# Kernel optimization log

Hardware: AMD Instinct MI355X
Metric: run time of the kernel (lower is better)

## Reference

```python
import jax, jax.numpy as jnp
import numpy as np

NUM_CLASSES = 10


def _decode(out, thresh, anchors, stride):
    # out: [B, 45, H, W] -> [B, H, W, 3, 15]
    B, C, H, W = out.shape
    o = out.transpose(0, 2, 3, 1).reshape(B, H, W, 3, -1)
    mask = o[..., 0] > thresh                      # [B,H,W,3]
    ys = jnp.arange(H, dtype=o.dtype)[None, :, None, None]
    xs = jnp.arange(W, dtype=o.dtype)[None, None, :, None]
    pre_x = (xs + o[..., 1]) * stride
    pre_y = (ys + o[..., 2]) * stride
    iou = o[..., 0]
    kind = jnp.argmax(o[..., 5:5 + NUM_CLASSES], axis=-1).astype(o.dtype)
    pre_w = anchors[:, 0] * jnp.exp(o[..., 3])     # anchors broadcast over last (anchor) dim
    pre_h = anchors[:, 1] * jnp.exp(o[..., 4])
    x1 = pre_x - 0.5 * pre_w
    y1 = pre_y - 0.5 * pre_h
    x2 = pre_x + 0.5 * pre_w
    y2 = pre_y + 0.5 * pre_h
    boxes = jnp.stack([iou, x1, y1, x2, y2, kind], axis=-1)  # [B,H,W,3,6]
    return boxes.reshape(-1, 6), mask.reshape(-1)


def setup_inputs() -> dict:
    key = jax.random.key(0)
    k = jax.random.split(key, 6)
    return {
        "output13": jax.random.normal(k[0], (128, 45, 13, 13), dtype=jnp.float32),
        "output26": jax.random.normal(k[1], (128, 45, 26, 26), dtype=jnp.float32),
        "output52": jax.random.normal(k[2], (128, 45, 52, 52), dtype=jnp.float32),
        "anchors13": jax.random.uniform(k[3], (3, 2), dtype=jnp.float32),
        "anchors26": jax.random.uniform(k[4], (3, 2), dtype=jnp.float32),
        "anchors52": jax.random.uniform(k[5], (3, 2), dtype=jnp.float32),
        "thresh": jnp.zeros((), dtype=jnp.float32),
    }


def reference(output13, output26, output52, anchors13, anchors26, anchors52, thresh):
    # JIT-friendly dense equivalent of mask -> nonzero -> gather -> decode:
    # decode every (batch, cell, anchor) slot and return the compaction mask
    # alongside; the masked rows correspond exactly to torch's gathered rows.
    b13, m13 = _decode(output13, thresh, anchors13, 32.0)
    b26, m26 = _decode(output26, thresh, anchors26, 16.0)
    b52, m52 = _decode(output52, thresh, anchors52, 8.0)
    boxes = jnp.concatenate([b13, b26, b52], axis=0)  # [N_total, 6]
    mask = jnp.concatenate([m13, m26, m52], axis=0)   # [N_total]
    return boxes, mask
```

## Files before the change

### kernel.cpp

```cpp
#include <hip/hip_runtime.h>


constexpr int  BATCH = 128;
constexpr long N13 = 128L * 13 * 13 * 3;
constexpr long N26 = 128L * 26 * 26 * 3;
constexpr long N52 = 128L * 52 * 52 * 3;
constexpr long NTOT = N13 + N26 + N52;

constexpr int BLOCK = 256;
constexpr int T52 = 128 * 3 * (52 * 52 / 4);
constexpr int T26 = 128 * 3 * (26 * 26 / 4);
constexpr int T13 = (int)N13;
constexpr int B52 = (T52 + BLOCK - 1) / BLOCK;
constexpr int B26 = (T26 + BLOCK - 1) / BLOCK;
constexpr int B13 = (T13 + BLOCK - 1) / BLOCK;

template <int H, int STRIDE, long ROWOFF>
__device__ __forceinline__ void decode_vec(const float* __restrict__ o,
                                           const float* __restrict__ anc,
                                           float thresh,
                                           float* __restrict__ out, int tid)
{
    constexpr int hw = H * H;
    constexpr int C4 = hw / 4;
    constexpr int NT = BATCH * 3 * C4;
    if (tid >= NT) return;

    int a = tid % 3;
    int t = tid / 3;
    int chunk = t % C4;
    int b = t / C4;

    const float4* base = (const float4*)o + (b * 45 + a * 15) * C4 + chunk;

    float v[15][4];
#pragma unroll
    for (int j = 0; j < 15; ++j) {
        float4 q = base[j * C4];
        v[j][0] = q.x; v[j][1] = q.y; v[j][2] = q.z; v[j][3] = q.w;
    }

    float2 A = ((const float2*)anc)[a];

    int cell0 = chunk * 4;
    int x = cell0 % H;
    int y = cell0 / H;
    long row = ROWOFF + ((long)b * hw + cell0) * 3 + a;

#pragma unroll
    for (int i = 0; i < 4; ++i) {
        float iou = v[0][i];
        float px = ((float)x + v[1][i]) * (float)STRIDE;
        float py = ((float)y + v[2][i]) * (float)STRIDE;
        float pw = A.x * expf(v[3][i]);
        float ph = A.y * expf(v[4][i]);

        int kind = 0;
        float best = v[5][i];
#pragma unroll
        for (int c = 1; c < 10; ++c)
            if (v[5 + c][i] > best) { best = v[5 + c][i]; kind = c; }

        float2* orow = (float2*)out + row * 3;
        orow[0] = make_float2(iou, px - 0.5f * pw);
        orow[1] = make_float2(py - 0.5f * ph, px + 0.5f * pw);
        orow[2] = make_float2(py + 0.5f * ph, (float)kind);
        out[6 * NTOT + row] = (iou > thresh) ? 1.0f : 0.0f;

        row += 3;
        if (++x == H) { x = 0; ++y; }
    }
}

template <int H, int STRIDE, long ROWOFF>
__device__ __forceinline__ void decode_scalar(const float* __restrict__ o,
                                              const float* __restrict__ anc,
                                              float thresh,
                                              float* __restrict__ out, int tid)
{
    constexpr int hw = H * H;
    constexpr int NT = BATCH * hw * 3;
    if (tid >= NT) return;

    int a = tid % 3;
    int cell = tid / 3;
    int x = (cell % hw) % H;
    int y = (cell % hw) / H;
    int b = cell / hw;

    const float* p = o + (b * 45 + a * 15) * hw + y * H + x;

    float v[15];
#pragma unroll
    for (int j = 0; j < 15; ++j) v[j] = p[j * hw];

    float iou = v[0];
    float px = ((float)x + v[1]) * (float)STRIDE;
    float py = ((float)y + v[2]) * (float)STRIDE;
    float2 A = ((const float2*)anc)[a];
    float pw = A.x * expf(v[3]);
    float ph = A.y * expf(v[4]);

    int kind = 0;
    float best = v[5];
#pragma unroll
    for (int c = 1; c < 10; ++c)
        if (v[5 + c] > best) { best = v[5 + c]; kind = c; }

    long row = ROWOFF + tid;
    float2* orow = (float2*)out + row * 3;
    orow[0] = make_float2(iou, px - 0.5f * pw);
    orow[1] = make_float2(py - 0.5f * ph, px + 0.5f * pw);
    orow[2] = make_float2(py + 0.5f * ph, (float)kind);
    out[6 * NTOT + row] = (iou > thresh) ? 1.0f : 0.0f;
}

__global__ __launch_bounds__(256) void decode_all(
    const float* __restrict__ o13, const float* __restrict__ o26,
    const float* __restrict__ o52, const float* __restrict__ a13,
    const float* __restrict__ a26, const float* __restrict__ a52,
    const float* __restrict__ thr, float* __restrict__ out)
{
    const float thresh = *thr;
    int blk = blockIdx.x;
    if (blk < B52) {
        decode_vec<52, 8, N13 + N26>(o52, a52, thresh, out, blk * BLOCK + (int)threadIdx.x);
    } else if (blk < B52 + B26) {
        decode_vec<26, 16, N13>(o26, a26, thresh, out, (blk - B52) * BLOCK + (int)threadIdx.x);
    } else {
        decode_scalar<13, 32, 0L>(o13, a13, thresh, out, (blk - B52 - B26) * BLOCK + (int)threadIdx.x);
    }
}

extern "C" void kernel_launch(void* const* d_in, const int* in_sizes, int n_in,
                              void* d_out, int out_size, void* d_ws, size_t ws_size,
                              hipStream_t stream) {
    const float* o13 = (const float*)d_in[0];
    const float* o26 = (const float*)d_in[1];
    const float* o52 = (const float*)d_in[2];
    const float* a13 = (const float*)d_in[3];
    const float* a26 = (const float*)d_in[4];
    const float* a52 = (const float*)d_in[5];
    const float* thr = (const float*)d_in[6];
    float* out = (float*)d_out;

    decode_all<<<B52 + B26 + B13, BLOCK, 0, stream>>>(o13, o26, o52, a13, a26, a52, thr, out);
}
```

Measured before the change: 137.0 us.

## Stage decoded boxes in LDS and write them out with coalesced float4 stores

Each 192-thread block now covers 64 consecutive 4-cell chunks across all 3 anchors, with one wavefront per anchor. Boxes and mask values are staged in shared memory and then written back as contiguous float4 stores. This replaces the strided float2 and scalar global writes of the old layout. It adds a __syncthreads and about 21 KB of LDS per block, which may limit occupancy, and changes the block size and grid mapping so every block divides the problem exactly.

Result: faster. 126.7 us (-7.5%).

```diff
diff --git a/kernel.cpp b/kernel.cpp
--- a/kernel.cpp
+++ b/kernel.cpp
@@ -7,45 +7,47 @@
 constexpr long N52 = 128L * 52 * 52 * 3;
 constexpr long NTOT = N13 + N26 + N52;
 
-constexpr int BLOCK = 256;
-constexpr int T52 = 128 * 3 * (52 * 52 / 4);
-constexpr int T26 = 128 * 3 * (26 * 26 / 4);
-constexpr int T13 = (int)N13;
-constexpr int B52 = (T52 + BLOCK - 1) / BLOCK;
-constexpr int B26 = (T26 + BLOCK - 1) / BLOCK;
-constexpr int B13 = (T13 + BLOCK - 1) / BLOCK;
+constexpr int BLOCK = 192;
+constexpr int GC52 = 128 * (52 * 52 / 4);
+constexpr int GC26 = 128 * (26 * 26 / 4);
+constexpr int B52 = GC52 / 64;
+constexpr int B26 = GC26 / 64;
+constexpr int B13 = (int)N13 / BLOCK;
 
 template <int H, int STRIDE, long ROWOFF>
-__device__ __forceinline__ void decode_vec(const float* __restrict__ o,
-                                           const float* __restrict__ anc,
-                                           float thresh,
-                                           float* __restrict__ out, int tid)
+__device__ __forceinline__ void decode_vec_lds(const float* __restrict__ o,
+                                               const float* __restrict__ anc,
+                                               float thresh,
+                                               float* __restrict__ out, int blk)
 {
     constexpr int hw = H * H;
     constexpr int C4 = hw / 4;
-    constexpr int NT = BATCH * 3 * C4;
-    if (tid >= NT) return;
 
-    int a = tid % 3;
-    int t = tid / 3;
-    int chunk = t % C4;
-    int b = t / C4;
+    __shared__ float sbox[768 * 6];
+    __shared__ float smask[768];
 
-    const float4* base = (const float4*)o + (b * 45 + a * 15) * C4 + chunk;
+    const int lane = threadIdx.x & 63;
+    const int a    = threadIdx.x >> 6;
+    const int gc0  = blk * 64;
+    const int gc   = gc0 + lane;
+    const int b    = gc / C4;
+    const int chunk = gc % C4;
+
+    const float4* base = (const float4*)o + (long)(b * 45 + a * 15) * C4 + chunk;
 
     float v[15][4];
 #pragma unroll
     for (int j = 0; j < 15; ++j) {
-        float4 q = base[j * C4];
+        float4 q = base[(long)j * C4];
         v[j][0] = q.x; v[j][1] = q.y; v[j][2] = q.z; v[j][3] = q.w;
     }
 
-    float2 A = ((const float2*)anc)[a];
+    const float2 A = ((const float2*)anc)[a];
 
     int cell0 = chunk * 4;
     int x = cell0 % H;
     int y = cell0 / H;
-    long row = ROWOFF + ((long)b * hw + cell0) * 3 + a;
+    int lr = lane * 12 + a;
 
 #pragma unroll
     for (int i = 0; i < 4; ++i) {
@@ -61,15 +63,26 @@
         for (int c = 1; c < 10; ++c)
             if (v[5 + c][i] > best) { best = v[5 + c][i]; kind = c; }
 
-        float2* orow = (float2*)out + row * 3;
-        orow[0] = make_float2(iou, px - 0.5f * pw);
-        orow[1] = make_float2(py - 0.5f * ph, px + 0.5f * pw);
-        orow[2] = make_float2(py + 0.5f * ph, (float)kind);
-        out[6 * NTOT + row] = (iou > thresh) ? 1.0f : 0.0f;
+        float* r = &sbox[(lr + i * 3) * 6];
+        ((float2*)r)[0] = make_float2(iou, px - 0.5f * pw);
+        ((float2*)r)[1] = make_float2(py - 0.5f * ph, px + 0.5f * pw);
+        ((float2*)r)[2] = make_float2(py + 0.5f * ph, (float)kind);
+        smask[lr + i * 3] = (iou > thresh) ? 1.0f : 0.0f;
 
-        row += 3;
         if (++x == H) { x = 0; ++y; }
     }
+
+    __syncthreads();
+
+    const long row0 = ROWOFF + (long)gc0 * 12;
+    const float4* sb = (const float4*)sbox;
+    float4* ob = (float4*)(out + row0 * 6);
+#pragma unroll
+    for (int k = 0; k < 6; ++k)
+        ob[threadIdx.x + k * BLOCK] = sb[threadIdx.x + k * BLOCK];
+
+    float4* om = (float4*)(out + 6 * NTOT + row0);
+    om[threadIdx.x] = ((const float4*)smask)[threadIdx.x];
 }
 
 template <int H, int STRIDE, long ROWOFF>
@@ -79,8 +92,6 @@
                                               float* __restrict__ out, int tid)
 {
     constexpr int hw = H * H;
-    constexpr int NT = BATCH * hw * 3;
-    if (tid >= NT) return;
 
     int a = tid % 3;
     int cell = tid / 3;
@@ -115,7 +126,7 @@
     out[6 * NTOT + row] = (iou > thresh) ? 1.0f : 0.0f;
 }
 
-__global__ __launch_bounds__(256) void decode_all(
+__global__ __launch_bounds__(BLOCK) void decode_all(
     const float* __restrict__ o13, const float* __restrict__ o26,
     const float* __restrict__ o52, const float* __restrict__ a13,
     const float* __restrict__ a26, const float* __restrict__ a52,
@@ -124,11 +135,12 @@
     const float thresh = *thr;
     int blk = blockIdx.x;
     if (blk < B52) {
-        decode_vec<52, 8, N13 + N26>(o52, a52, thresh, out, blk * BLOCK + (int)threadIdx.x);
+        decode_vec_lds<52, 8, N13 + N26>(o52, a52, thresh, out, blk);
     } else if (blk < B52 + B26) {
-        decode_vec<26, 16, N13>(o26, a26, thresh, out, (blk - B52) * BLOCK + (int)threadIdx.x);
+        decode_vec_lds<26, 16, N13>(o26, a26, thresh, out, blk - B52);
     } else {
-        decode_scalar<13, 32, 0L>(o13, a13, thresh, out, (blk - B52 - B26) * BLOCK + (int)threadIdx.x);
+        decode_scalar<13, 32, 0L>(o13, a13, thresh, out,
+                                  (blk - B52 - B26) * BLOCK + (int)threadIdx.x);
     }
 }
 
```
